# Kernel optimization log

Hardware: AMD Instinct MI355X
Metric: run time of the kernel (lower is better)

The kernel has to match this reference:

```python
import jax, jax.numpy as jnp
import numpy as np

B, N, E, F, H = 8, 20000, 640000, 8, 128


def setup_inputs() -> dict:
    key = jax.random.key(0)
    ks = jax.random.split(key, 8)
    x = jax.random.normal(ks[0], (B, N, F), dtype=jnp.float32)
    edge_index = jax.random.randint(ks[1], (B, 2, E), 0, N, dtype=jnp.int64)
    node_idx = jax.random.randint(ks[2], (B,), 0, N, dtype=jnp.int64)
    W1 = jax.random.normal(ks[3], (F, H), dtype=jnp.float32) / np.sqrt(F)
    W2 = jax.random.normal(ks[4], (H, H), dtype=jnp.float32) / np.sqrt(H)
    W3 = jax.random.normal(ks[5], (H, H), dtype=jnp.float32) / np.sqrt(H)
    Wl = jax.random.normal(ks[6], (H, 2), dtype=jnp.float32) / np.sqrt(H)
    return {
        "x": x, "edge_index": edge_index, "node_idx": node_idx,
        "W1": W1, "b1": jnp.zeros((H,), jnp.float32),
        "W2": W2, "b2": jnp.zeros((H,), jnp.float32),
        "W3": W3, "b3": jnp.zeros((H,), jnp.float32),
        "Wl": Wl, "bl": jnp.zeros((2,), jnp.float32),
    }


def _gcn_conv(x, edge_index, W, b):
    # PyG GCNConv: h = x W; out = D^{-1/2}(A+I)D^{-1/2} h + b  (self-loops added)
    n = x.shape[0]
    h = x @ W  # [N, H]
    src, dst = edge_index[0], edge_index[1]
    ones = jnp.ones(src.shape[0], dtype=x.dtype)
    deg = jax.ops.segment_sum(ones, dst, num_segments=n) + 1.0  # +1 for self-loop
    dinv = jax.lax.rsqrt(deg)  # [N]
    coef = dinv[src] * dinv[dst]  # [E]
    agg = jax.ops.segment_sum(h[src] * coef[:, None], dst, num_segments=n)
    agg = agg + h * (dinv * dinv)[:, None]  # self-loop contribution
    return agg + b


def _per_graph(x, edge_index, node_idx, W1, b1, W2, b2, W3, b3, Wl, bl):
    h = jax.nn.relu(_gcn_conv(x, edge_index, W1, b1))
    h = jax.nn.relu(h @ W2 + b2)
    h = jax.nn.relu(h @ W3 + b3)
    # dropout is identity in eval mode
    logits = h @ Wl + bl  # [N, 2]
    return logits[node_idx].flatten()  # [2]


def reference(x, edge_index, node_idx, W1, b1, W2, b2, W3, b3, Wl, bl):
    f = jax.vmap(_per_graph, in_axes=(0, 0, 0, None, None, None, None, None, None, None, None))
    return f(x, edge_index, node_idx, W1, b1, W2, b2, W3, b3, Wl, bl)  # [B, 2]
```

## Files before the change

### kernel.cpp

```cpp
#include <hip/hip_runtime.h>

#define NB 8
#define NN 20000
#define NE 640000
#define NF 8
#define NH 128
#define VPG (NE / 4)
#define WPG 64
#define NBLK (NB * WPG)
#define CHUNK_V (VPG / WPG)
#define SLOT 32
#define HW (NN / 4)
#define CAP 256
#define CAP1 (CAP + 1)

#define FLAGA_MAG 0x5A7BC0DEull
#define FLAGB_VAL 0xD00DFEEDC0FFEE42ull

#define WS_FLAGA_OFF 0
#define WS_FLAGB_OFF (NBLK * 8)
#define WS_LSTA_OFF  (WS_FLAGB_OFF + NBLK * 8)
#define WS_DEGP_OFF  (WS_LSTA_OFF + NBLK * SLOT * 4)

__device__ __forceinline__ void st32a(int* p, int v) {
    __hip_atomic_store(p, v, __ATOMIC_RELAXED, __HIP_MEMORY_SCOPE_AGENT);
}
__device__ __forceinline__ int ld32a(int* p) {
    return __hip_atomic_load(p, __ATOMIC_RELAXED, __HIP_MEMORY_SCOPE_AGENT);
}
__device__ __forceinline__ void st64a(unsigned long long* p, unsigned long long v) {
    __hip_atomic_store(p, v, __ATOMIC_RELAXED, __HIP_MEMORY_SCOPE_AGENT);
}
__device__ __forceinline__ unsigned long long ld64a(unsigned long long* p) {
    return __hip_atomic_load(p, __ATOMIC_RELAXED, __HIP_MEMORY_SCOPE_AGENT);
}

__global__ __launch_bounds__(256) void fused_gcn(
    const float* __restrict__ x, const int* __restrict__ ei,
    const int* __restrict__ nidx,
    const float* __restrict__ W1, const float* __restrict__ b1,
    const float* __restrict__ W2, const float* __restrict__ b2,
    const float* __restrict__ W3, const float* __restrict__ b3,
    const float* __restrict__ Wl, const float* __restrict__ bl,
    unsigned long long* __restrict__ flagA, unsigned long long* __restrict__ flagB,
    int* __restrict__ lstA, int* __restrict__ degp,
    float* __restrict__ out)
{
    const int bid = blockIdx.x, b = bid / WPG, w = bid % WPG;
    const int tid = threadIdx.x;
    const int bbase = b * WPG;
    const int tgt = nidx[b];

    const int* dstp = ei + (size_t)b * 2 * NE + NE;
    const int* srcp = ei + (size_t)b * 2 * NE;
    const int start = w * CHUNK_V;

    __shared__ unsigned histo[HW];
    __shared__ int sc[256];
    __shared__ int carr[WPG], coff[WPG], cs[WPG];
    __shared__ int ntot;
    __shared__ int compact[CAP];
    __shared__ int degT[CAP1];
    __shared__ float dinv[CAP1];
    __shared__ float pp[2 * NH];
    __shared__ float h1[NH], h2[NH], h3[NH];

    for (int i = tid; i < HW; i += 256) histo[i] = 0u;
    __syncthreads();

    unsigned long long mmask = 0ull;
    {
        int it = 0;
        for (int v = start + tid; v < start + CHUNK_V; v += 256, ++it) {
            int4 d = ((const int4*)dstp)[v];
            int dd[4] = {d.x, d.y, d.z, d.w};
            unsigned m4 = 0u;
#pragma unroll
            for (int c = 0; c < 4; ++c) {
                atomicAdd(&histo[dd[c] >> 2], 1u << ((dd[c] & 3) * 8));
                m4 |= (dd[c] == tgt ? 1u : 0u) << c;
            }
            mmask |= (unsigned long long)m4 << (it * 4);
        }
    }
    const int mycnt = __popcll(mmask);
    sc[tid] = mycnt;
    __syncthreads();
#pragma unroll
    for (int d = 1; d < 256; d <<= 1) {
        int v = sc[tid];
        if (tid >= d) v += sc[tid - d];
        __syncthreads();
        sc[tid] = v;
        __syncthreads();
    }
    {
        int base = sc[tid] - mycnt;
        unsigned long long mm = mmask;
        while (mm) {
            int bit = __ffsll(mm) - 1; mm &= mm - 1;
            int it2 = bit >> 2, c = bit & 3;
            int e = 4 * (start + tid + it2 * 256) + c;
            if (base < SLOT) st32a(&lstA[(bbase + w) * SLOT + base], srcp[e]);
            ++base;
        }
    }
    int mtot = sc[255]; if (mtot > SLOT) mtot = SLOT;
    asm volatile("s_waitcnt vmcnt(0)" ::: "memory");
    __syncthreads();
    if (tid == 0)
        st64a(&flagA[bbase + w], (FLAGA_MAG << 32) | (unsigned)mtot);

    if (tid < WPG) {
        unsigned long long f;
        while (((f = ld64a(&flagA[bbase + tid])) >> 32) != FLAGA_MAG)
            __builtin_amdgcn_s_sleep(2);
        carr[tid] = (int)(f & 0xFFFFFFFFull);
        cs[tid] = carr[tid];
    }
    __syncthreads();
#pragma unroll
    for (int d = 1; d < WPG; d <<= 1) {
        int v = 0;
        if (tid < WPG) { v = cs[tid]; if (tid >= d) v += cs[tid - d]; }
        __syncthreads();
        if (tid < WPG) cs[tid] = v;
        __syncthreads();
    }
    if (tid < WPG) coff[tid] = cs[tid] - carr[tid];
    if (tid == 0) ntot = cs[WPG - 1];
    __syncthreads();
    int n = ntot; if (n > CAP) n = CAP;
    for (int idx = tid; idx < WPG * SLOT; idx += 256) {
        int w2 = idx >> 5, s = idx & 31;
        if (s < carr[w2]) {
            int pos = coff[w2] + s;
            if (pos < CAP) compact[pos] = ld32a(&lstA[(bbase + w2) * SLOT + s]);
        }
    }
    __syncthreads();
    for (int i = tid; i <= n; i += 256) {
        int node = (i == n) ? tgt : compact[i];
        unsigned pw = histo[node >> 2];
        int dgr = (int)((pw >> ((node & 3) * 8)) & 0xFFu);
        st32a(&degp[((size_t)b * CAP1 + i) * WPG + w], dgr);
    }
    asm volatile("s_waitcnt vmcnt(0)" ::: "memory");
    __syncthreads();
    if (tid == 0) st64a(&flagB[bbase + w], FLAGB_VAL);
    if (w != 0) return;

    if (tid < WPG) {
        while (ld64a(&flagB[bbase + tid]) != FLAGB_VAL)
            __builtin_amdgcn_s_sleep(2);
    }
    __syncthreads();
    for (int i = tid; i <= n; i += 256) degT[i] = 0;
    __syncthreads();
    for (int idx = tid; idx < (n + 1) * 2; idx += 256) {
        int i = idx >> 1, g = idx & 1;
        int* row = &degp[((size_t)b * CAP1 + i) * WPG];
        int s = 0;
#pragma unroll
        for (int k = 0; k < 32; ++k) s += ld32a(&row[g * 32 + k]);
        atomicAdd(&degT[i], s);
    }
    __syncthreads();
    for (int i = tid; i <= n; i += 256)
        dinv[i] = rsqrtf((float)(degT[i] + 1));
    __syncthreads();

    const float* xb = x + (size_t)b * NN * NF;
    const float dt = dinv[n];
    const int j = tid & (NH - 1);
    const int half = tid >> 7;

    {
        float acc = 0.f;
        for (int i = half; i <= n; i += 2) {
            int s = (i == n) ? tgt : compact[i];
            float coef = (i == n) ? dt * dt : dinv[i] * dt;
            const float* xs = xb + (size_t)s * NF;
            float hs = 0.f;
#pragma unroll
            for (int k = 0; k < NF; ++k) hs += xs[k] * W1[k * NH + j];
            acc += hs * coef;
        }
        pp[half * NH + j] = acc;
    }
    __syncthreads();
    if (tid < NH) { float v = pp[j] + pp[NH + j] + b1[j]; h1[j] = v > 0.f ? v : 0.f; }
    __syncthreads();
    {
        float a = 0.f;
        const int k0 = half * 64;
#pragma unroll 8
        for (int k = k0; k < k0 + 64; ++k) a += h1[k] * W2[k * NH + j];
        pp[half * NH + j] = a;
    }
    __syncthreads();
    if (tid < NH) { float v = pp[j] + pp[NH + j] + b2[j]; h2[j] = v > 0.f ? v : 0.f; }
    __syncthreads();
    {
        float a = 0.f;
        const int k0 = half * 64;
#pragma unroll 8
        for (int k = k0; k < k0 + 64; ++k) a += h2[k] * W3[k * NH + j];
        pp[half * NH + j] = a;
    }
    __syncthreads();
    if (tid < NH) { float v = pp[j] + pp[NH + j] + b3[j]; h3[j] = v > 0.f ? v : 0.f; }
    __syncthreads();
    if (tid < 2) {
        float o = bl[tid];
        for (int k = 0; k < NH; ++k) o += h3[k] * Wl[k * 2 + tid];
        out[b * 2 + tid] = o;
    }
}

extern "C" void kernel_launch(void* const* d_in, const int* in_sizes, int n_in,
                              void* d_out, int out_size, void* d_ws, size_t ws_size,
                              hipStream_t stream) {
    const float* x    = (const float*)d_in[0];
    const int*   ei   = (const int*)d_in[1];
    const int*   nidx = (const int*)d_in[2];
    const float* W1 = (const float*)d_in[3];
    const float* b1 = (const float*)d_in[4];
    const float* W2 = (const float*)d_in[5];
    const float* b2 = (const float*)d_in[6];
    const float* W3 = (const float*)d_in[7];
    const float* b3 = (const float*)d_in[8];
    const float* Wl = (const float*)d_in[9];
    const float* bl = (const float*)d_in[10];
    float* out = (float*)d_out;

    char* ws = (char*)d_ws;
    unsigned long long* flagA = (unsigned long long*)(ws + WS_FLAGA_OFF);
    unsigned long long* flagB = (unsigned long long*)(ws + WS_FLAGB_OFF);
    int* lstA = (int*)(ws + WS_LSTA_OFF);
    int* degp = (int*)(ws + WS_DEGP_OFF);

    fused_gcn<<<NBLK, 256, 0, stream>>>(x, ei, nidx, W1, b1, W2, b2,
                                        W3, b3, Wl, bl,
                                        flagA, flagB, lstA, degp, out);
}
```

Measured before the change: 28.55 us.

## Replace LDS barrier scans with wave shuffles and add dedicated finisher blocks

The 256-wide and 64-wide Hillis-Steele prefix scans, which needed many __syncthreads, become wavefront __shfl_up scans combined with per-wave totals. The per-graph tail work (degree reduction, gather, MLP) moves from block w==0 into NB extra blocks launched after the worker blocks, which spin on the flags. Worker blocks now only count and publish. This cuts barrier overhead, but the finisher blocks rely on co-residency with the workers for the spin-waits and also repeat the compaction work themselves.

```diff
diff --git a/kernel.cpp b/kernel.cpp
--- a/kernel.cpp
+++ b/kernel.cpp
@@ -46,18 +46,12 @@
     int* __restrict__ lstA, int* __restrict__ degp,
     float* __restrict__ out)
 {
-    const int bid = blockIdx.x, b = bid / WPG, w = bid % WPG;
-    const int tid = threadIdx.x;
-    const int bbase = b * WPG;
-    const int tgt = nidx[b];
-
-    const int* dstp = ei + (size_t)b * 2 * NE + NE;
-    const int* srcp = ei + (size_t)b * 2 * NE;
-    const int start = w * CHUNK_V;
+    const int tid  = threadIdx.x;
+    const int lane = tid & 63, wv = tid >> 6;
 
     __shared__ unsigned histo[HW];
-    __shared__ int sc[256];
-    __shared__ int carr[WPG], coff[WPG], cs[WPG];
+    __shared__ int wtot[4];
+    __shared__ int carr[WPG], coff[WPG];
     __shared__ int ntot;
     __shared__ int compact[CAP];
     __shared__ int degT[CAP1];
@@ -65,70 +59,121 @@
     __shared__ float pp[2 * NH];
     __shared__ float h1[NH], h2[NH], h3[NH];
 
-    for (int i = tid; i < HW; i += 256) histo[i] = 0u;
-    __syncthreads();
-
-    unsigned long long mmask = 0ull;
-    {
-        int it = 0;
-        for (int v = start + tid; v < start + CHUNK_V; v += 256, ++it) {
-            int4 d = ((const int4*)dstp)[v];
-            int dd[4] = {d.x, d.y, d.z, d.w};
-            unsigned m4 = 0u;
-#pragma unroll
-            for (int c = 0; c < 4; ++c) {
-                atomicAdd(&histo[dd[c] >> 2], 1u << ((dd[c] & 3) * 8));
-                m4 |= (dd[c] == tgt ? 1u : 0u) << c;
-            }
-            mmask |= (unsigned long long)m4 << (it * 4);
-        }
-    }
-    const int mycnt = __popcll(mmask);
-    sc[tid] = mycnt;
-    __syncthreads();
-#pragma unroll
-    for (int d = 1; d < 256; d <<= 1) {
-        int v = sc[tid];
-        if (tid >= d) v += sc[tid - d];
-        __syncthreads();
-        sc[tid] = v;
-        __syncthreads();
-    }
-    {
-        int base = sc[tid] - mycnt;
-        unsigned long long mm = mmask;
-        while (mm) {
-            int bit = __ffsll(mm) - 1; mm &= mm - 1;
-            int it2 = bit >> 2, c = bit & 3;
-            int e = 4 * (start + tid + it2 * 256) + c;
-            if (base < SLOT) st32a(&lstA[(bbase + w) * SLOT + base], srcp[e]);
-            ++base;
-        }
-    }
-    int mtot = sc[255]; if (mtot > SLOT) mtot = SLOT;
-    asm volatile("s_waitcnt vmcnt(0)" ::: "memory");
-    __syncthreads();
-    if (tid == 0)
-        st64a(&flagA[bbase + w], (FLAGA_MAG << 32) | (unsigned)mtot);
+    if (blockIdx.x < NBLK) {
+        const int bid = blockIdx.x, b = bid / WPG, w = bid % WPG;
+        const int bbase = b * WPG;
+        const int tgt = nidx[b];
+        const int* dstp = ei + (size_t)b * 2 * NE + NE;
+        const int* srcp = ei + (size_t)b * 2 * NE;
+        const int start = w * CHUNK_V;
+
+        for (int i = tid; i < HW; i += 256) histo[i] = 0u;
+        __syncthreads();
+
+        unsigned long long mmask = 0ull;
+        {
+            int it = 0;
+            for (int v = start + tid; v < start + CHUNK_V; v += 256, ++it) {
+                int4 d = ((const int4*)dstp)[v];
+                int dd[4] = {d.x, d.y, d.z, d.w};
+                unsigned m4 = 0u;
+#pragma unroll
+                for (int c = 0; c < 4; ++c) {
+                    atomicAdd(&histo[dd[c] >> 2], 1u << ((dd[c] & 3) * 8));
+                    m4 |= (dd[c] == tgt ? 1u : 0u) << c;
+                }
+                mmask |= (unsigned long long)m4 << (it * 4);
+            }
+        }
+        const int mycnt = __popcll(mmask);
+        int v = mycnt;
+#pragma unroll
+        for (int d = 1; d < 64; d <<= 1) {
+            int o = __shfl_up(v, d, 64);
+            if (lane >= d) v += o;
+        }
+        if (lane == 63) wtot[wv] = v;
+        __syncthreads();
+        int wo = 0;
+        for (int i = 0; i < wv; ++i) wo += wtot[i];
+        {
+            int base = v + wo - mycnt;
+            unsigned long long mm = mmask;
+            while (mm) {
+                int bit = __ffsll(mm) - 1; mm &= mm - 1;
+                int it2 = bit >> 2, c = bit & 3;
+                int e = 4 * (start + tid + it2 * 256) + c;
+                if (base < SLOT) st32a(&lstA[(bbase + w) * SLOT + base], srcp[e]);
+                ++base;
+            }
+        }
+        int mtot = wtot[0] + wtot[1] + wtot[2] + wtot[3];
+        if (mtot > SLOT) mtot = SLOT;
+        asm volatile("s_waitcnt vmcnt(0)" ::: "memory");
+        __syncthreads();
+        if (tid == 0)
+            st64a(&flagA[bbase + w], (FLAGA_MAG << 32) | (unsigned)mtot);
+
+        if (tid < WPG) {
+            unsigned long long f;
+            while (((f = ld64a(&flagA[bbase + tid])) >> 32) != FLAGA_MAG)
+                __builtin_amdgcn_s_sleep(2);
+            carr[tid] = (int)(f & 0xFFFFFFFFull);
+        }
+        if (tid < WPG) {
+            int cv = carr[tid];
+            int s = cv;
+#pragma unroll
+            for (int d = 1; d < WPG; d <<= 1) {
+                int o = __shfl_up(s, d, 64);
+                if (lane >= d) s += o;
+            }
+            coff[tid] = s - cv;
+            if (tid == WPG - 1) ntot = s;
+        }
+        __syncthreads();
+        int n = ntot; if (n > CAP) n = CAP;
+        for (int idx = tid; idx < WPG * SLOT; idx += 256) {
+            int w2 = idx >> 5, s = idx & 31;
+            if (s < carr[w2]) {
+                int pos = coff[w2] + s;
+                if (pos < CAP) compact[pos] = ld32a(&lstA[(bbase + w2) * SLOT + s]);
+            }
+        }
+        __syncthreads();
+        for (int i = tid; i <= n; i += 256) {
+            int node = (i == n) ? tgt : compact[i];
+            unsigned pw = histo[node >> 2];
+            int dgr = (int)((pw >> ((node & 3) * 8)) & 0xFFu);
+            st32a(&degp[((size_t)b * CAP1 + i) * WPG + w], dgr);
+        }
+        asm volatile("s_waitcnt vmcnt(0)" ::: "memory");
+        __syncthreads();
+        if (tid == 0) st64a(&flagB[bbase + w], FLAGB_VAL);
+        return;
+    }
+
+    const int b = blockIdx.x - NBLK;
+    const int bbase = b * WPG;
+    const int tgt = nidx[b];
 
     if (tid < WPG) {
         unsigned long long f;
         while (((f = ld64a(&flagA[bbase + tid])) >> 32) != FLAGA_MAG)
             __builtin_amdgcn_s_sleep(2);
         carr[tid] = (int)(f & 0xFFFFFFFFull);
-        cs[tid] = carr[tid];
-    }
-    __syncthreads();
-#pragma unroll
-    for (int d = 1; d < WPG; d <<= 1) {
-        int v = 0;
-        if (tid < WPG) { v = cs[tid]; if (tid >= d) v += cs[tid - d]; }
-        __syncthreads();
-        if (tid < WPG) cs[tid] = v;
-        __syncthreads();
-    }
-    if (tid < WPG) coff[tid] = cs[tid] - carr[tid];
-    if (tid == 0) ntot = cs[WPG - 1];
+    }
+    if (tid < WPG) {
+        int cv = carr[tid];
+        int s = cv;
+#pragma unroll
+        for (int d = 1; d < WPG; d <<= 1) {
+            int o = __shfl_up(s, d, 64);
+            if (lane >= d) s += o;
+        }
+        coff[tid] = s - cv;
+        if (tid == WPG - 1) ntot = s;
+    }
     __syncthreads();
     int n = ntot; if (n > CAP) n = CAP;
     for (int idx = tid; idx < WPG * SLOT; idx += 256) {
@@ -138,18 +183,6 @@
             if (pos < CAP) compact[pos] = ld32a(&lstA[(bbase + w2) * SLOT + s]);
         }
     }
-    __syncthreads();
-    for (int i = tid; i <= n; i += 256) {
-        int node = (i == n) ? tgt : compact[i];
-        unsigned pw = histo[node >> 2];
-        int dgr = (int)((pw >> ((node & 3) * 8)) & 0xFFu);
-        st32a(&degp[((size_t)b * CAP1 + i) * WPG + w], dgr);
-    }
-    asm volatile("s_waitcnt vmcnt(0)" ::: "memory");
-    __syncthreads();
-    if (tid == 0) st64a(&flagB[bbase + w], FLAGB_VAL);
-    if (w != 0) return;
-
     if (tid < WPG) {
         while (ld64a(&flagB[bbase + tid]) != FLAGB_VAL)
             __builtin_amdgcn_s_sleep(2);
@@ -189,7 +222,7 @@
         pp[half * NH + j] = acc;
     }
     __syncthreads();
-    if (tid < NH) { float v = pp[j] + pp[NH + j] + b1[j]; h1[j] = v > 0.f ? v : 0.f; }
+    if (tid < NH) { float v1 = pp[j] + pp[NH + j] + b1[j]; h1[j] = v1 > 0.f ? v1 : 0.f; }
     __syncthreads();
     {
         float a = 0.f;
@@ -199,7 +232,7 @@
         pp[half * NH + j] = a;
     }
     __syncthreads();
-    if (tid < NH) { float v = pp[j] + pp[NH + j] + b2[j]; h2[j] = v > 0.f ? v : 0.f; }
+    if (tid < NH) { float v2 = pp[j] + pp[NH + j] + b2[j]; h2[j] = v2 > 0.f ? v2 : 0.f; }
     __syncthreads();
     {
         float a = 0.f;
@@ -209,7 +242,7 @@
         pp[half * NH + j] = a;
     }
     __syncthreads();
-    if (tid < NH) { float v = pp[j] + pp[NH + j] + b3[j]; h3[j] = v > 0.f ? v : 0.f; }
+    if (tid < NH) { float v3 = pp[j] + pp[NH + j] + b3[j]; h3[j] = v3 > 0.f ? v3 : 0.f; }
     __syncthreads();
     if (tid < 2) {
         float o = bl[tid];
@@ -240,7 +273,7 @@
     int* lstA = (int*)(ws + WS_LSTA_OFF);
     int* degp = (int*)(ws + WS_DEGP_OFF);
 
-    fused_gcn<<<NBLK, 256, 0, stream>>>(x, ei, nidx, W1, b1, W2, b2,
-                                        W3, b3, Wl, bl,
-                                        flagA, flagB, lstA, degp, out);
-}
+    fused_gcn<<<NBLK + NB, 256, 0, stream>>>(x, ei, nidx, W1, b1, W2, b2,
+                                             W3, b3, Wl, bl,
+                                             flagA, flagB, lstA, degp, out);
+}
```

Measured after the change: 24.27 us. 15.0% less time.
